# Kernel tuning notes

Measured on AMD Instinct MI355X. Metric: run time of the kernel, lower is better.

## Reference

```python
import jax, jax.numpy as jnp
import numpy as np

S, B, D, E, F = 2048, 2, 1024, 8, 4096


def setup_inputs() -> dict:
    key = jax.random.key(0)
    ks = jax.random.split(key, 6)
    x = jax.random.normal(ks[0], (S, B, D), dtype=jnp.float32)
    w_switch = jax.random.normal(ks[1], (D, E), dtype=jnp.float32) / np.sqrt(D)
    b_switch = jnp.zeros((E,), dtype=jnp.float32)
    w1 = jax.random.normal(ks[2], (E, D, F), dtype=jnp.float32) / np.sqrt(D)
    b1 = jnp.zeros((E, F), dtype=jnp.float32)
    w2 = jax.random.normal(ks[3], (E, F, D), dtype=jnp.float32) / np.sqrt(F)
    b2 = jnp.zeros((E, D), dtype=jnp.float32)
    return {"x": x, "w_switch": w_switch, "b_switch": b_switch,
            "w1": w1, "b1": b1, "w2": w2, "b2": b2}


def reference(x, w_switch, b_switch, w1, b1, w2, b2):
    # x: [S, B, D] -> tokens [N, D]
    s, b, d = x.shape
    n_experts = w1.shape[0]
    xf = x.reshape(-1, d)                                    # [N, D]
    route_prob = jax.nn.softmax(xf @ w_switch + b_switch, axis=-1)  # [N, E]
    route_prob_max = jnp.max(route_prob, axis=-1)            # [N]
    routes = jnp.argmax(route_prob, axis=-1)                 # [N] int
    # is_scale_prob=True: scale token by its routing probability before FFN
    xs = xf * route_prob_max[:, None]                        # [N, D]
    # Per-expert FFN evaluated densely (drop_tokens=False => every token kept),
    # then each token selects its routed expert's output.
    h = jax.nn.relu(jnp.einsum('nd,edf->enf', xs, w1) + b1[:, None, :])  # [E, N, F]
    y = jnp.einsum('enf,efd->end', h, w2) + b2[:, None, :]               # [E, N, D]
    n = xf.shape[0]
    out = y[routes, jnp.arange(n)]                           # [N, D]
    counts = jnp.zeros((n_experts,), dtype=jnp.float32).at[routes].add(1.0)
    n_dropped = jnp.zeros((), dtype=jnp.int32)               # drop_tokens=False
    return out.reshape(s, b, d), counts, route_prob.sum(0), n_dropped
```

## Files before the change

kernel.cpp:

```cpp
#include <hip/hip_runtime.h>
#include <hip/hip_bf16.h>

#define NTOK 4096
#define DDIM 1024
#define NEXP 8
#define FDIM 4096
#define MAXTILES 40

typedef __attribute__((ext_vector_type(4))) float f32x4;
typedef __attribute__((ext_vector_type(8))) short bf16x8;
typedef __attribute__((ext_vector_type(8))) unsigned short u16x8;

#define GLDS(g, l) __builtin_amdgcn_global_load_lds( \
    (const __attribute__((address_space(1))) unsigned int*)(g), \
    (__attribute__((address_space(3))) unsigned int*)(l), 16, 0, 0)

__global__ __launch_bounds__(256) void route_kernel(
    const float* __restrict__ x,
    const float* __restrict__ w_switch,
    const float* __restrict__ b_switch,
    __hip_bfloat16* __restrict__ xs,
    int* __restrict__ amax_arr,
    float* __restrict__ partial)
{
    const int tid = threadIdx.x;
    const int wave = tid >> 6, lane = tid & 63;
    __shared__ float pr[4][16];

    float wacc[16];
#pragma unroll
    for (int j = 0; j < 16; j++) wacc[j] = 0.0f;

    for (int i = 0; i < 4; i++) {
        const int n = blockIdx.x * 16 + wave * 4 + i;
        const float4* xr = (const float4*)(x + (size_t)n * DDIM);
        float4 xv[4];
#pragma unroll
        for (int j = 0; j < 4; j++) xv[j] = xr[lane + j * 64];

        float acc[NEXP];
#pragma unroll
        for (int e = 0; e < NEXP; e++) acc[e] = 0.0f;
#pragma unroll
        for (int j = 0; j < 4; j++) {
            const int dbase = (lane + j * 64) * 4;
#pragma unroll
            for (int c = 0; c < 4; c++) {
                const float4* wr = (const float4*)(w_switch + (size_t)(dbase + c) * NEXP);
                float4 w0 = wr[0], w1 = wr[1];
                float xvc = ((const float*)&xv[j])[c];
                acc[0] += xvc * w0.x; acc[1] += xvc * w0.y;
                acc[2] += xvc * w0.z; acc[3] += xvc * w0.w;
                acc[4] += xvc * w1.x; acc[5] += xvc * w1.y;
                acc[6] += xvc * w1.z; acc[7] += xvc * w1.w;
            }
        }
#pragma unroll
        for (int e = 0; e < NEXP; e++) {
            float v = acc[e];
#pragma unroll
            for (int off = 32; off > 0; off >>= 1) v += __shfl_xor(v, off, 64);
            acc[e] = v;
        }
        float mx = -1e30f;
#pragma unroll
        for (int e = 0; e < NEXP; e++) {
            acc[e] += b_switch[e];
            mx = fmaxf(mx, acc[e]);
        }
        float sum = 0.0f;
#pragma unroll
        for (int e = 0; e < NEXP; e++) { acc[e] = __expf(acc[e] - mx); sum += acc[e]; }
        float inv = 1.0f / sum;
        float pmax = -1.0f; int amax = 0;
#pragma unroll
        for (int e = 0; e < NEXP; e++) {
            float p = acc[e] * inv;
            acc[e] = p;
            if (p > pmax) { pmax = p; amax = e; }
        }
#pragma unroll
        for (int e = 0; e < NEXP; e++) {
            wacc[e] += acc[e];
            wacc[8 + e] += (amax == e) ? 1.0f : 0.0f;
        }
        if (lane == 0) amax_arr[n] = amax;
#pragma unroll
        for (int j = 0; j < 4; j++) {
            ushort4 pk;
            __hip_bfloat16* pp = (__hip_bfloat16*)&pk;
            pp[0] = __float2bfloat16(xv[j].x * pmax);
            pp[1] = __float2bfloat16(xv[j].y * pmax);
            pp[2] = __float2bfloat16(xv[j].z * pmax);
            pp[3] = __float2bfloat16(xv[j].w * pmax);
            *(ushort4*)(xs + (size_t)n * DDIM + (lane + j * 64) * 4) = pk;
        }
    }
    if (lane == 0) {
#pragma unroll
        for (int j = 0; j < 16; j++) pr[wave][j] = wacc[j];
    }
    __syncthreads();
    if (tid < 16)
        partial[blockIdx.x * 16 + tid] = pr[0][tid] + pr[1][tid] + pr[2][tid] + pr[3][tid];
}

__global__ __launch_bounds__(1024) void bucket_kernel(
    const int* __restrict__ amax_arr, int* __restrict__ bucket, int* __restrict__ ecnt)
{
    const int e = blockIdx.x;
    __shared__ int ctr;
    if (threadIdx.x == 0) ctr = 0;
    __syncthreads();
    const int lane = threadIdx.x & 63;
    for (int c = 0; c < NTOK; c += 1024) {
        int t = c + threadIdx.x;
        bool my = (amax_arr[t] == e);
        unsigned long long mask = __ballot(my);
        int cnt = __popcll(mask);
        int base = 0;
        if (lane == 0 && cnt) base = atomicAdd(&ctr, cnt);
        base = __shfl(base, 0, 64);
        if (my) {
            int rank = __popcll(mask & ((1ull << lane) - 1ull));
            bucket[e * NTOK + base + rank] = t;
        }
    }
    __syncthreads();
    if (threadIdx.x == 0) ecnt[e] = ctr;
}

__global__ __launch_bounds__(256) void finalize_table_kernel(
    const float* __restrict__ partial, const int* __restrict__ ecnt,
    float* __restrict__ out_tail, int* __restrict__ table)
{
    __shared__ float red[16][16];
    const int j = threadIdx.x & 15, g = threadIdx.x >> 4;
    float s = 0.0f;
    for (int k = 0; k < 16; k++) s += partial[(size_t)(g + k * 16) * 16 + j];
    red[g][j] = s;
    __syncthreads();
    if (threadIdx.x < 16) {
        float t = 0.0f;
        for (int k = 0; k < 16; k++) t += red[k][threadIdx.x];
        int dst = (threadIdx.x < 8) ? (8 + threadIdx.x) : (threadIdx.x - 8);
        out_tail[dst] = t;
    }
    if (threadIdx.x == 16) out_tail[16] = 0.0f;
    if (threadIdx.x == 0) {
        int idx = 0;
        for (int e = 0; e < NEXP; e++) {
            int cnt = ecnt[e];
            for (int m0 = 0; m0 < cnt; m0 += 128) table[idx++] = (e << 16) | m0;
        }
        for (; idx < MAXTILES; idx++) table[idx] = -1;
    }
}

__global__ __launch_bounds__(256) void init_out_kernel(
    const float* __restrict__ b2, const int* __restrict__ amax_arr,
    float* __restrict__ out)
{
    const int t = blockIdx.x;
    const int e = amax_arr[t];
    const float4* br = (const float4*)(b2 + (size_t)e * DDIM);
    ((float4*)(out + (size_t)t * DDIM))[threadIdx.x] = br[threadIdx.x];
}

template <int R, int C>
__global__ __launch_bounds__(256) void transpose_kernel(
    const float* __restrict__ in, __hip_bfloat16* __restrict__ outp)
{
    const int e = blockIdx.z;
    const int r0 = blockIdx.y * 64, c0 = blockIdx.x * 64;
    __shared__ __hip_bfloat16 t[64 * 65];
    const int tid = threadIdx.x;
    const int ri = tid >> 4, c4 = (tid & 15) * 4;
    const float* src = in + ((size_t)e * R + r0) * C + c0;
#pragma unroll
    for (int rr = 0; rr < 4; rr++) {
        int r = ri + rr * 16;
        float4 v = *(const float4*)(src + (size_t)r * C + c4);
        t[r * 65 + c4 + 0] = __float2bfloat16(v.x);
        t[r * 65 + c4 + 1] = __float2bfloat16(v.y);
        t[r * 65 + c4 + 2] = __float2bfloat16(v.z);
        t[r * 65 + c4 + 3] = __float2bfloat16(v.w);
    }
    __syncthreads();
    const int co = tid >> 2, m = tid & 3;
    u16x8 v0, v1;
#pragma unroll
    for (int idx = 0; idx < 8; idx++)
        ((unsigned short*)&v0)[idx] = *(const unsigned short*)&t[(m * 16 + idx) * 65 + co];
#pragma unroll
    for (int idx = 0; idx < 8; idx++)
        ((unsigned short*)&v1)[idx] = *(const unsigned short*)&t[(m * 16 + idx + 8) * 65 + co];
    __hip_bfloat16* dst = outp + ((size_t)e * C + c0 + co) * R + r0 + m * 16;
    *(u16x8*)(dst) = v0;
    *(u16x8*)(dst + 8) = v1;
}

template <int MODE, int K, int NN, int KS>
__device__ __forceinline__ void gemm_body(
    const __hip_bfloat16* __restrict__ A,
    const __hip_bfloat16* __restrict__ Bt,
    const float* __restrict__ bias,
    const int* __restrict__ bucket,
    const int* __restrict__ ecnt,
    const int* __restrict__ table,
    void* __restrict__ Out)
{
    const int entry = table[blockIdx.y];
    if (entry < 0) return;
    const int e = entry >> 16;
    const int m0 = entry & 0xffff;
    const int cnt = ecnt[e];
    const int n0 = blockIdx.x * 128;
    const int kbase = (K / KS) * blockIdx.z;

    __shared__ __align__(16) __hip_bfloat16 Asm[128 * 32];
    __shared__ __align__(16) __hip_bfloat16 Bsm[128 * 32];
    __shared__ int toks[128];

    const int tid = threadIdx.x;
    if (tid < 128) {
        int r = m0 + tid;
        toks[tid] = bucket[e * NTOK + (r < cnt ? r : cnt - 1)];
    }
    __syncthreads();

    const int wave = tid >> 6, lane = tid & 63;
    const int r = lane & 15, kq = lane >> 4;
    const int g0 = 2 * wave, g1 = 2 * wave + 1;

    const __hip_bfloat16* pA0 = A + (size_t)toks[g0 * 16 + r] * K + kbase + kq * 8;
    const __hip_bfloat16* pA1 = A + (size_t)toks[g1 * 16 + r] * K + kbase + kq * 8;
    const __hip_bfloat16* pB0 = Bt + ((size_t)e * NN + n0 + g0 * 16 + r) * K + kbase + kq * 8;
    const __hip_bfloat16* pB1 = Bt + ((size_t)e * NN + n0 + g1 * 16 + r) * K + kbase + kq * 8;
    char* lA0 = (char*)Asm + g0 * 1024;
    char* lA1 = (char*)Asm + g1 * 1024;
    char* lB0 = (char*)Bsm + g0 * 1024;
    char* lB1 = (char*)Bsm + g1 * 1024;

    const int wm = wave & 1, wn = wave >> 1;
    f32x4 acc[4][4];
#pragma unroll
    for (int t = 0; t < 4; t++)
#pragma unroll
        for (int u = 0; u < 4; u++) acc[t][u] = (f32x4){0.f, 0.f, 0.f, 0.f};

    for (int k0 = 0; k0 < K / KS; k0 += 32) {
        GLDS(pA0, lA0); GLDS(pA1, lA1);
        GLDS(pB0, lB0); GLDS(pB1, lB1);
        pA0 += 32; pA1 += 32; pB0 += 32; pB1 += 32;
        __syncthreads();
        bf16x8 a[4], b[4];
#pragma unroll
        for (int t = 0; t < 4; t++)
            a[t] = *(const bf16x8*)((const char*)Asm + (wm * 4 + t) * 1024 + lane * 16);
#pragma unroll
        for (int u = 0; u < 4; u++)
            b[u] = *(const bf16x8*)((const char*)Bsm + (wn * 4 + u) * 1024 + lane * 16);
#pragma unroll
        for (int t = 0; t < 4; t++)
#pragma unroll
            for (int u = 0; u < 4; u++)
                acc[t][u] = __builtin_amdgcn_mfma_f32_16x16x32_bf16(a[t], b[u], acc[t][u], 0, 0, 0);
        __syncthreads();
    }

    const int quad = lane >> 4, l15 = lane & 15;
    float bv[4];
#pragma unroll
    for (int u = 0; u < 4; u++)
        bv[u] = (MODE == 0) ? bias[(size_t)e * NN + n0 + wn * 64 + u * 16 + l15] : 0.0f;
#pragma unroll
    for (int t = 0; t < 4; t++) {
#pragma unroll
        for (int rr = 0; rr < 4; rr++) {
            int row = wm * 64 + t * 16 + quad * 4 + rr;
            if (m0 + row < cnt) {
                int tok = toks[row];
#pragma unroll
                for (int u = 0; u < 4; u++) {
                    int col = n0 + wn * 64 + u * 16 + l15;
                    float v = acc[t][u][rr] + bv[u];
                    if (MODE == 0) {
                        v = fmaxf(v, 0.0f);
                        ((__hip_bfloat16*)Out)[(size_t)tok * NN + col] = __float2bfloat16(v);
                    } else {
                        unsafeAtomicAdd(&((float*)Out)[(size_t)tok * NN + col], v);
                    }
                }
            }
        }
    }
}

__global__ __launch_bounds__(256) void gemm_ffn1(
    const __hip_bfloat16* __restrict__ A, const __hip_bfloat16* __restrict__ Bt,
    const float* __restrict__ bias, const int* __restrict__ bucket,
    const int* __restrict__ ecnt, const int* __restrict__ table, void* __restrict__ Out)
{
    gemm_body<0, DDIM, FDIM, 1>(A, Bt, bias, bucket, ecnt, table, Out);
}

__global__ __launch_bounds__(256) void gemm_ffn2(
    const __hip_bfloat16* __restrict__ A, const __hip_bfloat16* __restrict__ Bt,
    const float* __restrict__ bias, const int* __restrict__ bucket,
    const int* __restrict__ ecnt, const int* __restrict__ table, void* __restrict__ Out)
{
    gemm_body<1, FDIM, DDIM, 2>(A, Bt, bias, bucket, ecnt, table, Out);
}

extern "C" void kernel_launch(void* const* d_in, const int* in_sizes, int n_in,
                              void* d_out, int out_size, void* d_ws, size_t ws_size,
                              hipStream_t stream) {
    const float* x        = (const float*)d_in[0];
    const float* w_switch = (const float*)d_in[1];
    const float* b_switch = (const float*)d_in[2];
    const float* w1       = (const float*)d_in[3];
    const float* b1       = (const float*)d_in[4];
    const float* w2       = (const float*)d_in[5];
    const float* b2       = (const float*)d_in[6];

    float* out = (float*)d_out;
    float* out_tail = out + (size_t)NTOK * DDIM;

    char* ws = (char*)d_ws;
    __hip_bfloat16* xs = (__hip_bfloat16*)(ws);
    __hip_bfloat16* h  = (__hip_bfloat16*)(ws + 8388608ull);
    __hip_bfloat16* wt = (__hip_bfloat16*)(ws + 41943040ull);
    int* bucket        = (int*)(ws + 109051904ull);
    int* amax_arr      = (int*)(ws + 109182976ull);
    float* partial     = (float*)(ws + 109199360ull);
    int* ecnt          = (int*)(ws + 109215744ull);
    int* table         = (int*)(ws + 109215776ull);

    hipLaunchKernelGGL(route_kernel, dim3(256), dim3(256), 0, stream,
                       x, w_switch, b_switch, xs, amax_arr, partial);
    hipLaunchKernelGGL(bucket_kernel, dim3(NEXP), dim3(1024), 0, stream,
                       amax_arr, bucket, ecnt);
    hipLaunchKernelGGL(finalize_table_kernel, dim3(1), dim3(256), 0, stream,
                       partial, ecnt, out_tail, table);
    hipLaunchKernelGGL(init_out_kernel, dim3(NTOK), dim3(256), 0, stream,
                       b2, amax_arr, out);

    hipLaunchKernelGGL((transpose_kernel<DDIM, FDIM>), dim3(FDIM / 64, DDIM / 64, NEXP),
                       dim3(256), 0, stream, w1, wt);
    hipLaunchKernelGGL(gemm_ffn1, dim3(FDIM / 128, MAXTILES), dim3(256), 0, stream,
                       xs, wt, b1, bucket, ecnt, table, (void*)h);

    hipLaunchKernelGGL((transpose_kernel<FDIM, DDIM>), dim3(DDIM / 64, FDIM / 64, NEXP),
                       dim3(256), 0, stream, w2, wt);
    hipLaunchKernelGGL(gemm_ffn2, dim3(DDIM / 128, MAXTILES, 2), dim3(256), 0, stream,
                       h, wt, b2, bucket, ecnt, table, (void*)out);
}
```

Baseline: 526.4 us.

## Double-buffer LDS tiles in expert GEMM to overlap loads with MFMA

Splits the A and B shared-memory tiles into two buffers. The next K-slice is issued with global_load_lds into the idle buffer while MFMAs run on the current one. Each step now ends with a single vmcnt wait and barrier instead of two __syncthreads, so global-load latency can overlap with compute. In exchange the tiles use twice the LDS, which may lower occupancy, and the wait still drains all loads before each barrier.

```diff
diff --git a/kernel.cpp b/kernel.cpp
--- a/kernel.cpp
+++ b/kernel.cpp
@@ -218,8 +218,8 @@
     const int n0 = blockIdx.x * 128;
     const int kbase = (K / KS) * blockIdx.z;
 
-    __shared__ __align__(16) __hip_bfloat16 Asm[128 * 32];
-    __shared__ __align__(16) __hip_bfloat16 Bsm[128 * 32];
+    __shared__ __align__(16) __hip_bfloat16 Asm[2][128 * 32];
+    __shared__ __align__(16) __hip_bfloat16 Bsm[2][128 * 32];
     __shared__ int toks[128];
 
     const int tid = threadIdx.x;
@@ -231,16 +231,14 @@
 
     const int wave = tid >> 6, lane = tid & 63;
     const int r = lane & 15, kq = lane >> 4;
-    const int g0 = 2 * wave, g1 = 2 * wave + 1;
+    const int g0 = 2 * wave;
 
     const __hip_bfloat16* pA0 = A + (size_t)toks[g0 * 16 + r] * K + kbase + kq * 8;
-    const __hip_bfloat16* pA1 = A + (size_t)toks[g1 * 16 + r] * K + kbase + kq * 8;
+    const __hip_bfloat16* pA1 = A + (size_t)toks[(g0 + 1) * 16 + r] * K + kbase + kq * 8;
     const __hip_bfloat16* pB0 = Bt + ((size_t)e * NN + n0 + g0 * 16 + r) * K + kbase + kq * 8;
-    const __hip_bfloat16* pB1 = Bt + ((size_t)e * NN + n0 + g1 * 16 + r) * K + kbase + kq * 8;
-    char* lA0 = (char*)Asm + g0 * 1024;
-    char* lA1 = (char*)Asm + g1 * 1024;
-    char* lB0 = (char*)Bsm + g0 * 1024;
-    char* lB1 = (char*)Bsm + g1 * 1024;
+    const __hip_bfloat16* pB1 = Bt + ((size_t)e * NN + n0 + (g0 + 1) * 16 + r) * K + kbase + kq * 8;
+    char* lA = (char*)Asm + g0 * 1024;
+    char* lB = (char*)Bsm + g0 * 1024;
 
     const int wm = wave & 1, wn = wave >> 1;
     f32x4 acc[4][4];
@@ -249,24 +247,41 @@
 #pragma unroll
         for (int u = 0; u < 4; u++) acc[t][u] = (f32x4){0.f, 0.f, 0.f, 0.f};
 
-    for (int k0 = 0; k0 < K / KS; k0 += 32) {
-        GLDS(pA0, lA0); GLDS(pA1, lA1);
-        GLDS(pB0, lB0); GLDS(pB1, lB1);
-        pA0 += 32; pA1 += 32; pB0 += 32; pB1 += 32;
-        __syncthreads();
+    constexpr int NSTEP = (K / KS) / 32;
+
+    GLDS(pA0, lA); GLDS(pA1, lA + 1024);
+    GLDS(pB0, lB); GLDS(pB1, lB + 1024);
+    pA0 += 32; pA1 += 32; pB0 += 32; pB1 += 32;
+    asm volatile("s_waitcnt vmcnt(0)" ::: "memory");
+    __builtin_amdgcn_s_barrier();
+
+    int cur = 0;
+    for (int t = 0; t < NSTEP; ++t) {
+        if (t + 1 < NSTEP) {
+            const int so = (cur ^ 1) * 8192;
+            GLDS(pA0, lA + so); GLDS(pA1, lA + so + 1024);
+            GLDS(pB0, lB + so); GLDS(pB1, lB + so + 1024);
+            pA0 += 32; pA1 += 32; pB0 += 32; pB1 += 32;
+        }
+        const char* Ab = (const char*)Asm + cur * 8192;
+        const char* Bb = (const char*)Bsm + cur * 8192;
         bf16x8 a[4], b[4];
 #pragma unroll
-        for (int t = 0; t < 4; t++)
-            a[t] = *(const bf16x8*)((const char*)Asm + (wm * 4 + t) * 1024 + lane * 16);
+        for (int t4 = 0; t4 < 4; t4++)
+            a[t4] = *(const bf16x8*)(Ab + (wm * 4 + t4) * 1024 + lane * 16);
 #pragma unroll
         for (int u = 0; u < 4; u++)
-            b[u] = *(const bf16x8*)((const char*)Bsm + (wn * 4 + u) * 1024 + lane * 16);
-#pragma unroll
-        for (int t = 0; t < 4; t++)
+            b[u] = *(const bf16x8*)(Bb + (wn * 4 + u) * 1024 + lane * 16);
+#pragma unroll
+        for (int t4 = 0; t4 < 4; t4++)
 #pragma unroll
             for (int u = 0; u < 4; u++)
-                acc[t][u] = __builtin_amdgcn_mfma_f32_16x16x32_bf16(a[t], b[u], acc[t][u], 0, 0, 0);
-        __syncthreads();
+                acc[t4][u] = __builtin_amdgcn_mfma_f32_16x16x32_bf16(a[t4], b[u], acc[t4][u], 0, 0, 0);
+        if (t + 1 < NSTEP) {
+            asm volatile("s_waitcnt vmcnt(0)" ::: "memory");
+            __builtin_amdgcn_s_barrier();
+        }
+        cur ^= 1;
     }
 
     const int quad = lane >> 4, l15 = lane & 15;
```

After: 536.3 us. No clear change (+1.9%).

## Remap GEMM grid to XCD-aware 1D ordering and fold b2 init into epilogue

Applied to the files above, without the earlier changes.

The 2D/3D GEMM grids become a 1D grid whose block index is decoded so that consecutive blocks on the same XCD share a routing tile (y = xcd + 8*yk). The intent is to keep the expert weight and token-tile reuse within one XCD's L2. The init_out kernel that wrote b2 rows is replaced by a memset plus adding b2 in the split-K z==0 epilogue. This removes one gather kernel, at the cost of a plain memset and a slightly more complex index decode.

```diff
diff --git a/kernel.cpp b/kernel.cpp
--- a/kernel.cpp
+++ b/kernel.cpp
@@ -157,16 +157,6 @@
     }
 }
 
-__global__ __launch_bounds__(256) void init_out_kernel(
-    const float* __restrict__ b2, const int* __restrict__ amax_arr,
-    float* __restrict__ out)
-{
-    const int t = blockIdx.x;
-    const int e = amax_arr[t];
-    const float4* br = (const float4*)(b2 + (size_t)e * DDIM);
-    ((float4*)(out + (size_t)t * DDIM))[threadIdx.x] = br[threadIdx.x];
-}
-
 template <int R, int C>
 __global__ __launch_bounds__(256) void transpose_kernel(
     const float* __restrict__ in, __hip_bfloat16* __restrict__ outp)
@@ -200,7 +190,7 @@
     *(u16x8*)(dst + 8) = v1;
 }
 
-template <int MODE, int K, int NN, int KS>
+template <int MODE, int K, int NN, int KS, int NX>
 __device__ __forceinline__ void gemm_body(
     const __hip_bfloat16* __restrict__ A,
     const __hip_bfloat16* __restrict__ Bt,
@@ -210,13 +200,21 @@
     const int* __restrict__ table,
     void* __restrict__ Out)
 {
-    const int entry = table[blockIdx.y];
+    const int bid = blockIdx.x;
+    const int xcd = bid & 7;
+    const int q = bid >> 3;
+    const int x = q % NX;
+    const int yk = (q / NX) % (MAXTILES / 8);
+    const int z = q / (NX * (MAXTILES / 8));
+    const int y = xcd + 8 * yk;
+
+    const int entry = table[y];
     if (entry < 0) return;
     const int e = entry >> 16;
     const int m0 = entry & 0xffff;
     const int cnt = ecnt[e];
-    const int n0 = blockIdx.x * 128;
-    const int kbase = (K / KS) * blockIdx.z;
+    const int n0 = x * 128;
+    const int kbase = (K / KS) * z;
 
     __shared__ __align__(16) __hip_bfloat16 Asm[128 * 32];
     __shared__ __align__(16) __hip_bfloat16 Bsm[128 * 32];
@@ -272,8 +270,12 @@
     const int quad = lane >> 4, l15 = lane & 15;
     float bv[4];
 #pragma unroll
-    for (int u = 0; u < 4; u++)
-        bv[u] = (MODE == 0) ? bias[(size_t)e * NN + n0 + wn * 64 + u * 16 + l15] : 0.0f;
+    for (int u = 0; u < 4; u++) {
+        if (MODE == 0)
+            bv[u] = bias[(size_t)e * NN + n0 + wn * 64 + u * 16 + l15];
+        else
+            bv[u] = (z == 0) ? bias[(size_t)e * NN + n0 + wn * 64 + u * 16 + l15] : 0.0f;
+    }
 #pragma unroll
     for (int t = 0; t < 4; t++) {
 #pragma unroll
@@ -302,7 +304,7 @@
     const float* __restrict__ bias, const int* __restrict__ bucket,
     const int* __restrict__ ecnt, const int* __restrict__ table, void* __restrict__ Out)
 {
-    gemm_body<0, DDIM, FDIM, 1>(A, Bt, bias, bucket, ecnt, table, Out);
+    gemm_body<0, DDIM, FDIM, 1, FDIM / 128>(A, Bt, bias, bucket, ecnt, table, Out);
 }
 
 __global__ __launch_bounds__(256) void gemm_ffn2(
@@ -310,7 +312,7 @@
     const float* __restrict__ bias, const int* __restrict__ bucket,
     const int* __restrict__ ecnt, const int* __restrict__ table, void* __restrict__ Out)
 {
-    gemm_body<1, FDIM, DDIM, 2>(A, Bt, bias, bucket, ecnt, table, Out);
+    gemm_body<1, FDIM, DDIM, 2, DDIM / 128>(A, Bt, bias, bucket, ecnt, table, Out);
 }
 
 extern "C" void kernel_launch(void* const* d_in, const int* in_sizes, int n_in,
@@ -337,22 +339,22 @@
     int* ecnt          = (int*)(ws + 109215744ull);
     int* table         = (int*)(ws + 109215776ull);
 
+    hipMemsetAsync(out, 0, (size_t)NTOK * DDIM * sizeof(float), stream);
+
     hipLaunchKernelGGL(route_kernel, dim3(256), dim3(256), 0, stream,
                        x, w_switch, b_switch, xs, amax_arr, partial);
     hipLaunchKernelGGL(bucket_kernel, dim3(NEXP), dim3(1024), 0, stream,
                        amax_arr, bucket, ecnt);
     hipLaunchKernelGGL(finalize_table_kernel, dim3(1), dim3(256), 0, stream,
                        partial, ecnt, out_tail, table);
-    hipLaunchKernelGGL(init_out_kernel, dim3(NTOK), dim3(256), 0, stream,
-                       b2, amax_arr, out);
 
     hipLaunchKernelGGL((transpose_kernel<DDIM, FDIM>), dim3(FDIM / 64, DDIM / 64, NEXP),
                        dim3(256), 0, stream, w1, wt);
-    hipLaunchKernelGGL(gemm_ffn1, dim3(FDIM / 128, MAXTILES), dim3(256), 0, stream,
+    hipLaunchKernelGGL(gemm_ffn1, dim3((FDIM / 128) * MAXTILES), dim3(256), 0, stream,
                        xs, wt, b1, bucket, ecnt, table, (void*)h);
 
     hipLaunchKernelGGL((transpose_kernel<FDIM, DDIM>), dim3(DDIM / 64, FDIM / 64, NEXP),
                        dim3(256), 0, stream, w2, wt);
-    hipLaunchKernelGGL(gemm_ffn2, dim3(DDIM / 128, MAXTILES, 2), dim3(256), 0, stream,
+    hipLaunchKernelGGL(gemm_ffn2, dim3((DDIM / 128) * MAXTILES * 2), dim3(256), 0, stream,
                        h, wt, b2, bucket, ecnt, table, (void*)out);
 }
```

After: 515.3 us. 2.1% less time.
